# Kernel tuning notes

Measured on AMD Instinct MI355X. Metric: run time of the kernel, lower is better.

The kernel has to match this reference:

```python
import jax, jax.numpy as jnp
import numpy as np

HEAD_DIM = 64
N_HEADS = 12
ROPE_BASE = 10000.0


def _rope_tables(seq_len, head_dim, dtype=jnp.float32):
    half = head_dim // 2
    inv_freq = 1.0 / (ROPE_BASE ** (jnp.arange(0, half, dtype=jnp.float32) / half))
    pos = jnp.arange(seq_len, dtype=jnp.float32)
    freqs = pos[:, None] * inv_freq[None, :]  # (s, half)
    return jnp.cos(freqs).astype(dtype), jnp.sin(freqs).astype(dtype)


def _apply_rope(t, cos, sin):
    # t: (b, h, s, d); rotate-half convention on full head_dim (rope_fraction=1.0)
    d = t.shape[-1]
    t1, t2 = t[..., : d // 2], t[..., d // 2 :]
    cos = cos[None, None, :, :]
    sin = sin[None, None, :, :]
    return jnp.concatenate([t1 * cos - t2 * sin, t1 * sin + t2 * cos], axis=-1)


def setup_inputs() -> dict:
    key = jax.random.key(0)
    ks = jax.random.split(key, 6)
    b, s, d_model = 16, 512, 768
    x = jax.random.normal(ks[0], (b, s, d_model), dtype=jnp.float32)
    chain_ids = jax.random.randint(ks[1], (b, s), 0, 2, dtype=jnp.int32)
    attention_mask = jnp.ones((b, s), dtype=bool)
    inner = N_HEADS * HEAD_DIM
    scale = 0.02
    Wq = jax.random.normal(ks[2], (d_model, inner), dtype=jnp.float32) * scale
    Wk = jax.random.normal(ks[3], (d_model, inner), dtype=jnp.float32) * scale
    Wv = jax.random.normal(ks[4], (d_model, inner), dtype=jnp.float32) * scale
    Wo = jax.random.normal(ks[5], (inner, d_model), dtype=jnp.float32) * scale
    return {"x": x, "chain_ids": chain_ids, "attention_mask": attention_mask,
            "Wq": Wq, "Wk": Wk, "Wv": Wv, "Wo": Wo}


def reference(x, chain_ids, attention_mask, Wq, Wk, Wv, Wo):
    b, s, _ = x.shape
    h, d = N_HEADS, HEAD_DIM
    scale = d ** (-0.5)

    def proj(W):
        return jnp.einsum('bse,ef->bsf', x, W).reshape(b, s, h, d).transpose(0, 2, 1, 3)

    q = proj(Wq)  # (b, h, s, d)
    k = proj(Wk)
    v = proj(Wv)

    cos, sin = _rope_tables(s, d, x.dtype)
    q_rope = _apply_rope(q, cos, sin)
    k_rope = _apply_rope(k, cos, sin)

    scores_intra = jnp.einsum('bhsd,bhtd->bhst', q_rope, k_rope) * scale
    scores_inter = jnp.einsum('bhsd,bhtd->bhst', q, k) * scale

    # intra-chain mask (b, 1, s, s)
    intra = (chain_ids[:, None, :, None] == chain_ids[:, None, None, :])
    merged = jnp.where(intra, scores_intra, scores_inter)

    # additive padding mask (b, 1, 1, s)
    pad = jnp.where(attention_mask[:, None, None, :], 0.0, -jnp.inf).astype(x.dtype)
    merged = merged + pad

    attn = jax.nn.softmax(merged, axis=-1)
    attn = jnp.nan_to_num(attn, nan=0.0)

    out = jnp.einsum('bhst,bhtd->bhsd', attn, v)
    out = out.transpose(0, 2, 1, 3).reshape(b, s, h * d)
    return jnp.einsum('bsf,fe->bse', out, Wo)
```

## Files before the change

### kernel.cpp

```cpp
#include <hip/hip_runtime.h>
#include <stdint.h>
#include <math.h>

#define NB 16
#define NS 512
#define NH 12
#define ND 64
#define NE 768
#define NF 768

typedef __attribute__((ext_vector_type(4))) float  f32x4;
typedef __attribute__((ext_vector_type(8))) short  bf16x8;
typedef __attribute__((ext_vector_type(4))) short  bf16x4;

__device__ __forceinline__ short f2bf(float f) {
    unsigned u = __builtin_bit_cast(unsigned, f);
    u += 0x7FFFu + ((u >> 16) & 1u);
    return (short)(u >> 16);
}
__device__ __forceinline__ float bf2f(short s) {
    unsigned u = ((unsigned)(unsigned short)s) << 16;
    return __builtin_bit_cast(float, u);
}

#define MFMA16(a, b, c) __builtin_amdgcn_mfma_f32_16x16x32_bf16((a), (b), (c), 0, 0, 0)

__device__ __forceinline__ bf16x8 lds_rd8(const short* base, int row, int cb) {
    return *(const bf16x8*)((const char*)base + (((row) * 128 + (cb)) ^ (((row) & 7) << 4)));
}

__global__ __launch_bounds__(256) void mask_probe_kernel(const unsigned char* __restrict__ m,
                                                         int* __restrict__ flag) {
    __shared__ int any;
    if (threadIdx.x == 0) any = 0;
    __syncthreads();
    int acc = 0;
    for (int i = threadIdx.x; i < NB * NS; i += 256) {
        if ((i & 3) && m[i]) acc = 1;
    }
    if (acc) atomicOr(&any, 1);
    __syncthreads();
    if (threadIdx.x == 0) *flag = any;
}

__global__ __launch_bounds__(256) void rope_table_kernel(float* __restrict__ cos_t,
                                                         float* __restrict__ sin_t) {
    int i = blockIdx.x * 256 + threadIdx.x;
    if (i >= NS * 32) return;
    int p = i >> 5;
    int j = i & 31;
    float inv_freq = powf(10000.0f, -(float)j / 32.0f);
    float ang = (float)p * inv_freq;
    cos_t[i] = cosf(ang);
    sin_t[i] = sinf(ang);
}

__global__ __launch_bounds__(256) void convert_x_kernel(const float* __restrict__ x,
                                                        short* __restrict__ xb) {
    int i = (blockIdx.x * 256 + threadIdx.x) * 8;
    if (i >= 8192 * 768) return;
    float4 a = *(const float4*)&x[i];
    float4 b = *(const float4*)&x[i + 4];
    bf16x8 r = { f2bf(a.x), f2bf(a.y), f2bf(a.z), f2bf(a.w),
                 f2bf(b.x), f2bf(b.y), f2bf(b.z), f2bf(b.w) };
    *(bf16x8*)&xb[i] = r;
}

__global__ __launch_bounds__(256) void convert_wt_kernel(
    const float* __restrict__ Wq, const float* __restrict__ Wk,
    const float* __restrict__ Wv, const float* __restrict__ Wo,
    short* __restrict__ Wqt, short* __restrict__ Wkt,
    short* __restrict__ Wvt, short* __restrict__ Wot) {
    const float* W  = (blockIdx.z == 0) ? Wq  : (blockIdx.z == 1) ? Wk  : (blockIdx.z == 2) ? Wv  : Wo;
    short*       Wt = (blockIdx.z == 0) ? Wqt : (blockIdx.z == 1) ? Wkt : (blockIdx.z == 2) ? Wvt : Wot;
    const int k0 = blockIdx.y * 64, n0 = blockIdx.x * 64;
    __shared__ float t[64][65];
    for (int u = threadIdx.x; u < 4096; u += 256) {
        int r = u >> 6, c = u & 63;
        t[r][c] = W[(size_t)(k0 + r) * 768 + n0 + c];
    }
    __syncthreads();
    for (int u = threadIdx.x; u < 4096; u += 256) {
        int c = u >> 6, r = u & 63;
        Wt[(size_t)(n0 + c) * 768 + k0 + r] = f2bf(t[r][c]);
    }
}

__global__ __launch_bounds__(256) void gemm_qkv_kernel(const short* __restrict__ xb,
    const short* __restrict__ Wqt, const short* __restrict__ Wkt, const short* __restrict__ Wvt,
    short* __restrict__ qo, short* __restrict__ ko, short* __restrict__ vo) {
    const int z = blockIdx.z;
    const short* Bt = (z == 0) ? Wqt : (z == 1) ? Wkt : Wvt;
    short*       O  = (z == 0) ? qo  : (z == 1) ? ko  : vo;
    const int n0 = blockIdx.x * 128, m0 = blockIdx.y * 128;
    __shared__ short As[128 * 64], Bs[128 * 64];
    const int tid = threadIdx.x, lane = tid & 63, wave = tid >> 6;
    const int g = lane >> 4, l15 = lane & 15;
    const int wm = wave >> 1, wn = wave & 1;
    f32x4 acc[4][4];
    #pragma unroll
    for (int i = 0; i < 4; ++i)
        #pragma unroll
        for (int j = 0; j < 4; ++j) acc[i][j] = (f32x4){0.f, 0.f, 0.f, 0.f};

    for (int kt = 0; kt < 12; ++kt) {
        __syncthreads();
        const short* Asrc = xb + (size_t)m0 * 768 + kt * 64;
        const short* Bsrc = Bt + (size_t)n0 * 768 + kt * 64;
        #pragma unroll
        for (int p = 0; p < 4; ++p) {
            int u = tid + p * 256;
            int row = u >> 3, slot = u & 7;
            int off = (row * 128 + slot * 16) ^ ((row & 7) << 4);
            *(bf16x8*)((char*)As + off) = *(const bf16x8*)(Asrc + (size_t)row * 768 + slot * 8);
            *(bf16x8*)((char*)Bs + off) = *(const bf16x8*)(Bsrc + (size_t)row * 768 + slot * 8);
        }
        __syncthreads();
        #pragma unroll
        for (int h2 = 0; h2 < 2; ++h2) {
            bf16x8 af[4], bfr[4];
            const int cb = h2 * 64 + g * 16;
            #pragma unroll
            for (int i = 0; i < 4; ++i) {
                af[i]  = lds_rd8(As, wm * 64 + i * 16 + l15, cb);
                bfr[i] = lds_rd8(Bs, wn * 64 + i * 16 + l15, cb);
            }
            #pragma unroll
            for (int i = 0; i < 4; ++i)
                #pragma unroll
                for (int j = 0; j < 4; ++j)
                    acc[i][j] = MFMA16(af[i], bfr[j], acc[i][j]);
        }
    }
    #pragma unroll
    for (int i = 0; i < 4; ++i)
        #pragma unroll
        for (int r = 0; r < 4; ++r) {
            int m = m0 + wm * 64 + i * 16 + g * 4 + r;
            int bb = m >> 9, ss = m & 511;
            #pragma unroll
            for (int j = 0; j < 4; ++j) {
                int n = n0 + wn * 64 + j * 16 + l15;
                int hh = n >> 6, dd = n & 63;
                O[(((size_t)bb * NH + hh) * NS + ss) * ND + dd] = f2bf(acc[i][j][r]);
            }
        }
}

__global__ __launch_bounds__(256) void v_tr_kernel(const short* __restrict__ v,
                                                   short* __restrict__ vt) {
    const int b = blockIdx.z, h = blockIdx.y, s0 = blockIdx.x * 64;
    const size_t base = (((size_t)b * NH + h) * NS + s0) * ND;
    const int tid = threadIdx.x;
    __shared__ short tv[64 * 72];
    #pragma unroll
    for (int p = 0; p < 2; ++p) {
        int u = tid + p * 256;
        int s = u >> 3, d8 = (u & 7) * 8;
        bf16x8 vv = *(const bf16x8*)(v + base + s * 64 + d8);
        #pragma unroll
        for (int j = 0; j < 8; ++j) tv[(d8 + j) * 72 + s] = vv[j];
    }
    __syncthreads();
    const size_t vtb = ((size_t)b * NH + h) * ND * NS + s0;
    #pragma unroll
    for (int p = 0; p < 2; ++p) {
        int u = tid + p * 256;
        int d = u >> 3, s8 = (u & 7) * 8;
        bf16x8 o = *(const bf16x8*)&tv[d * 72 + s8];
        *(bf16x8*)(vt + vtb + (size_t)d * NS + s8) = o;
    }
}

__global__ __launch_bounds__(256) void attn_fused_kernel(
    const short* __restrict__ qr, const short* __restrict__ kr, const short* __restrict__ vt,
    const float* __restrict__ cos_t, const float* __restrict__ sin_t,
    const int* __restrict__ chain, const void* __restrict__ amask,
    const int* __restrict__ mflag, short* __restrict__ aout) {
    const int lid = blockIdx.x;
    const int xcd = lid & 7;
    const int idx = lid >> 3;
    const int qt  = idx & 3;
    const int bh  = xcd * 24 + (idx >> 2);
    const int b = bh / 12, h = bh - (bh / 12) * 12;
    const int q0 = qt * 128;

    __shared__ short SM[20480];
    short* Kr_s = SM;
    short* Kp_s = SM + 4096;
    short* Vt_s = SM + 8192;
    __shared__ __align__(16) int   ck_s[64];
    __shared__ __align__(16) float kb_s[64];

    const int tid = threadIdx.x, lane = tid & 63, wave = tid >> 6;
    const int g = lane >> 4, l15 = lane & 15;
    const int m_u8 = *mflag;
    const size_t bhNS = (size_t)bh * NS;
    char* pb = (char*)(SM + 12288) + wave * 4096;

    const short* qrs = qr + (bhNS + q0) * ND;
    #pragma unroll
    for (int p = 0; p < 4; ++p) {
        int u = tid + p * 256;
        int row = u >> 3, slot = u & 7;
        int off = (row * 128 + slot * 16) ^ ((row & 7) << 4);
        *(bf16x8*)((char*)SM + off) = *(const bf16x8*)(qrs + row * 64 + slot * 8);
    }
    __syncthreads();
    bf16x8 fqr[2][2], fqp[2][2];
    int   cqv[2];
    #pragma unroll
    for (int qg = 0; qg < 2; ++qg) {
        int rrow = wave * 32 + qg * 16 + l15;
        fqr[qg][0] = lds_rd8(SM, rrow, g * 16);
        fqr[qg][1] = lds_rd8(SM, rrow, 64 + g * 16);
        int pos = q0 + rrow;
        float4 c0 = *(const float4*)&cos_t[pos * 32 + g * 8];
        float4 c1 = *(const float4*)&cos_t[pos * 32 + g * 8 + 4];
        float4 s0 = *(const float4*)&sin_t[pos * 32 + g * 8];
        float4 s1 = *(const float4*)&sin_t[pos * 32 + g * 8 + 4];
        float cc[8] = {c0.x, c0.y, c0.z, c0.w, c1.x, c1.y, c1.z, c1.w};
        float ss[8] = {s0.x, s0.y, s0.z, s0.w, s1.x, s1.y, s1.z, s1.w};
        #pragma unroll
        for (int j = 0; j < 8; ++j) {
            float t1 = bf2f(fqr[qg][0][j]), t2 = bf2f(fqr[qg][1][j]);
            fqp[qg][0][j] = f2bf(t1 * cc[j] - t2 * ss[j]);
            fqp[qg][1][j] = f2bf(t1 * ss[j] + t2 * cc[j]);
        }
        cqv[qg] = chain[b * NS + pos];
    }

    float m_run[2] = {-INFINITY, -INFINITY};
    float l_run[2] = {0.f, 0.f};
    f32x4 accO[2][4];
    #pragma unroll
    for (int qg = 0; qg < 2; ++qg)
        #pragma unroll
        for (int t = 0; t < 4; ++t) accO[qg][t] = (f32x4){0.f, 0.f, 0.f, 0.f};

    const short* krb = kr + bhNS * ND;
    const short* vtb = vt + bhNS * ND;

    for (int kv = 0; kv < 8; ++kv) {
        const int k0s = kv * 64;
        __syncthreads();
        {
            int key = tid >> 2, d8 = (tid & 3) * 8;
            const short* krow = krb + (k0s + key) * 64;
            bf16x8 lo = *(const bf16x8*)(krow + d8);
            bf16x8 hi = *(const bf16x8*)(krow + 32 + d8);
            float4 c0 = *(const float4*)&cos_t[(k0s + key) * 32 + d8];
            float4 c1 = *(const float4*)&cos_t[(k0s + key) * 32 + d8 + 4];
            float4 s0 = *(const float4*)&sin_t[(k0s + key) * 32 + d8];
            float4 s1 = *(const float4*)&sin_t[(k0s + key) * 32 + d8 + 4];
            float cc[8] = {c0.x, c0.y, c0.z, c0.w, c1.x, c1.y, c1.z, c1.w};
            float ss[8] = {s0.x, s0.y, s0.z, s0.w, s1.x, s1.y, s1.z, s1.w};
            bf16x8 plo, phi;
            #pragma unroll
            for (int j = 0; j < 8; ++j) {
                float t1 = bf2f(lo[j]), t2 = bf2f(hi[j]);
                plo[j] = f2bf(t1 * cc[j] - t2 * ss[j]);
                phi[j] = f2bf(t1 * ss[j] + t2 * cc[j]);
            }
            int basebyte = key * 128 + d8 * 2;
            int sw = (key & 7) << 4;
            *(bf16x8*)((char*)Kr_s + ((basebyte) ^ sw))      = lo;
            *(bf16x8*)((char*)Kr_s + ((basebyte + 64) ^ sw)) = hi;
            *(bf16x8*)((char*)Kp_s + ((basebyte) ^ sw))      = plo;
            *(bf16x8*)((char*)Kp_s + ((basebyte + 64) ^ sw)) = phi;
        }
        #pragma unroll
        for (int p = 0; p < 2; ++p) {
            int u = tid + p * 256;
            int d = u >> 3, s8 = (u & 7) * 8;
            bf16x8 vv = *(const bf16x8*)(vtb + (size_t)d * NS + k0s + s8);
            *(bf16x8*)((char*)Vt_s + ((d * 128 + s8 * 2) ^ ((d & 7) << 4))) = vv;
        }
        if (tid < 64) {
            int gidx = b * NS + k0s + tid;
            ck_s[tid] = chain[gidx];
            int ok = m_u8 ? (int)((const unsigned char*)amask)[gidx] : ((const int*)amask)[gidx];
            kb_s[tid] = ok ? 0.f : -INFINITY;
        }
        __syncthreads();

        float pm[2][4][4];
        float tmax[2] = {-INFINITY, -INFINITY};
        #pragma unroll
        for (int t = 0; t < 4; ++t) {
            bf16x8 akr0 = lds_rd8(Kr_s, t * 16 + l15, g * 16);
            bf16x8 akr1 = lds_rd8(Kr_s, t * 16 + l15, 64 + g * 16);
            bf16x8 akp0 = lds_rd8(Kp_s, t * 16 + l15, g * 16);
            bf16x8 akp1 = lds_rd8(Kp_s, t * 16 + l15, 64 + g * 16);
            int4   ck4 = *(const int4*)&ck_s[t * 16 + g * 4];
            float4 kb4 = *(const float4*)&kb_s[t * 16 + g * 4];
            const int   ckk[4] = {ck4.x, ck4.y, ck4.z, ck4.w};
            const float kbb[4] = {kb4.x, kb4.y, kb4.z, kb4.w};
            #pragma unroll
            for (int qg = 0; qg < 2; ++qg) {
                f32x4 sr = (f32x4){0.f, 0.f, 0.f, 0.f};
                f32x4 sp = (f32x4){0.f, 0.f, 0.f, 0.f};
                sr = MFMA16(akr0, fqr[qg][0], sr);
                sr = MFMA16(akr1, fqr[qg][1], sr);
                sp = MFMA16(akp0, fqp[qg][0], sp);
                sp = MFMA16(akp1, fqp[qg][1], sp);
                #pragma unroll
                for (int r = 0; r < 4; ++r) {
                    float sv = (cqv[qg] == ckk[r]) ? sp[r] : sr[r];
                    sv = sv * 0.125f + kbb[r];
                    pm[qg][t][r] = sv;
                    tmax[qg] = fmaxf(tmax[qg], sv);
                }
            }
        }

        #pragma unroll
        for (int qg = 0; qg < 2; ++qg) {
            float tm = tmax[qg];
            tm = fmaxf(tm, __shfl_xor(tm, 16));
            tm = fmaxf(tm, __shfl_xor(tm, 32));
            float mnew = fmaxf(m_run[qg], tm);
            float fac, psum = 0.f;
            if (mnew == -INFINITY) {
                fac = 1.f;
                #pragma unroll
                for (int t = 0; t < 4; ++t)
                    #pragma unroll
                    for (int r = 0; r < 4; ++r) pm[qg][t][r] = 0.f;
            } else {
                fac = __expf(m_run[qg] - mnew);
                #pragma unroll
                for (int t = 0; t < 4; ++t)
                    #pragma unroll
                    for (int r = 0; r < 4; ++r) {
                        float p = __expf(pm[qg][t][r] - mnew);
                        pm[qg][t][r] = p;
                        psum += p;
                    }
            }
            psum += __shfl_xor(psum, 16);
            psum += __shfl_xor(psum, 32);
            l_run[qg] = l_run[qg] * fac + psum;
            m_run[qg] = mnew;

            int prow = qg * 16 + l15;
            int psw = (prow & 7) << 4;
            #pragma unroll
            for (int t = 0; t < 4; ++t) {
                bf16x4 pk = { f2bf(pm[qg][t][0]), f2bf(pm[qg][t][1]),
                              f2bf(pm[qg][t][2]), f2bf(pm[qg][t][3]) };
                *(bf16x4*)(pb + ((prow * 128 + t * 32 + g * 8) ^ psw)) = pk;
            }
            float f4[4];
            #pragma unroll
            for (int r = 0; r < 4; ++r) f4[r] = __shfl(fac, g * 4 + r);
            #pragma unroll
            for (int t = 0; t < 4; ++t) {
                f32x4 a = accO[qg][t];
                a[0] *= f4[0]; a[1] *= f4[1]; a[2] *= f4[2]; a[3] *= f4[3];
                accO[qg][t] = a;
            }
            bf16x8 pa0 = *(const bf16x8*)(pb + ((prow * 128 + g * 16) ^ psw));
            bf16x8 pa1 = *(const bf16x8*)(pb + ((prow * 128 + 64 + g * 16) ^ psw));
            #pragma unroll
            for (int dt = 0; dt < 4; ++dt) {
                bf16x8 vb0 = lds_rd8(Vt_s, dt * 16 + l15, g * 16);
                bf16x8 vb1 = lds_rd8(Vt_s, dt * 16 + l15, 64 + g * 16);
                accO[qg][dt] = MFMA16(pa0, vb0, accO[qg][dt]);
                accO[qg][dt] = MFMA16(pa1, vb1, accO[qg][dt]);
            }
        }
    }

    #pragma unroll
    for (int qg = 0; qg < 2; ++qg) {
        float inv[4];
        #pragma unroll
        for (int r = 0; r < 4; ++r) {
            float lv = __shfl(l_run[qg], g * 4 + r);
            inv[r] = (lv > 0.f) ? 1.f / lv : 0.f;
        }
        #pragma unroll
        for (int dt = 0; dt < 4; ++dt)
            #pragma unroll
            for (int r = 0; r < 4; ++r) {
                int row = b * NS + q0 + wave * 32 + qg * 16 + g * 4 + r;
                aout[(size_t)row * NF + h * ND + dt * 16 + l15] = f2bf(accO[qg][dt][r] * inv[r]);
            }
    }
}

__global__ __launch_bounds__(256) void gemm_out_kernel(const short* __restrict__ A,
    const short* __restrict__ Wot, float* __restrict__ out) {
    const int n0 = blockIdx.x * 128, m0 = blockIdx.y * 128;
    __shared__ short As[128 * 64], Bs[128 * 64];
    const int tid = threadIdx.x, lane = tid & 63, wave = tid >> 6;
    const int g = lane >> 4, l15 = lane & 15;
    const int wm = wave >> 1, wn = wave & 1;
    f32x4 acc[4][4];
    #pragma unroll
    for (int i = 0; i < 4; ++i)
        #pragma unroll
        for (int j = 0; j < 4; ++j) acc[i][j] = (f32x4){0.f, 0.f, 0.f, 0.f};

    for (int kt = 0; kt < 12; ++kt) {
        __syncthreads();
        const short* Asrc = A   + (size_t)m0 * 768 + kt * 64;
        const short* Bsrc = Wot + (size_t)n0 * 768 + kt * 64;
        #pragma unroll
        for (int p = 0; p < 4; ++p) {
            int u = tid + p * 256;
            int row = u >> 3, slot = u & 7;
            int off = (row * 128 + slot * 16) ^ ((row & 7) << 4);
            *(bf16x8*)((char*)As + off) = *(const bf16x8*)(Asrc + (size_t)row * 768 + slot * 8);
            *(bf16x8*)((char*)Bs + off) = *(const bf16x8*)(Bsrc + (size_t)row * 768 + slot * 8);
        }
        __syncthreads();
        #pragma unroll
        for (int h2 = 0; h2 < 2; ++h2) {
            bf16x8 af[4], bfr[4];
            const int cb = h2 * 64 + g * 16;
            #pragma unroll
            for (int i = 0; i < 4; ++i) {
                af[i]  = lds_rd8(As, wm * 64 + i * 16 + l15, cb);
                bfr[i] = lds_rd8(Bs, wn * 64 + i * 16 + l15, cb);
            }
            #pragma unroll
            for (int i = 0; i < 4; ++i)
                #pragma unroll
                for (int j = 0; j < 4; ++j)
                    acc[i][j] = MFMA16(af[i], bfr[j], acc[i][j]);
        }
    }
    #pragma unroll
    for (int i = 0; i < 4; ++i)
        #pragma unroll
        for (int r = 0; r < 4; ++r) {
            int m = m0 + wm * 64 + i * 16 + g * 4 + r;
            #pragma unroll
            for (int j = 0; j < 4; ++j) {
                int n = n0 + wn * 64 + j * 16 + l15;
                out[(size_t)m * NE + n] = acc[i][j][r];
            }
        }
}

extern "C" void kernel_launch(void* const* d_in, const int* in_sizes, int n_in,
                              void* d_out, int out_size, void* d_ws, size_t ws_size,
                              hipStream_t stream) {
    const float* x     = (const float*)d_in[0];
    const int*   chain = (const int*)d_in[1];
    const void*  amask = d_in[2];
    const float* Wq = (const float*)d_in[3];
    const float* Wk = (const float*)d_in[4];
    const float* Wv = (const float*)d_in[5];
    const float* Wo = (const float*)d_in[6];
    float* out = (float*)d_out;

    const size_t QSZ = (size_t)NB * NH * NS * ND;
    char* w = (char*)d_ws;
    float* cos_t = (float*)w;  w += (size_t)NS * 32 * 4;
    float* sin_t = (float*)w;  w += (size_t)NS * 32 * 4;
    int*   mflag = (int*)w;    w += 256;
    short* xb    = (short*)w;  w += (size_t)8192 * 768 * 2;
    short* Wqt   = (short*)w;  w += (size_t)768 * 768 * 2;
    short* Wkt   = (short*)w;  w += (size_t)768 * 768 * 2;
    short* Wvt   = (short*)w;  w += (size_t)768 * 768 * 2;
    short* Wot   = (short*)w;  w += (size_t)768 * 768 * 2;
    short* q_raw = (short*)w;  w += QSZ * 2;
    short* k_raw = (short*)w;  w += QSZ * 2;
    short* v_nat = (short*)w;  w += QSZ * 2;
    short* vtr   = (short*)w;  w += QSZ * 2;
    short* aout  = xb;

    mask_probe_kernel<<<dim3(1), dim3(256), 0, stream>>>((const unsigned char*)amask, mflag);
    rope_table_kernel<<<dim3(64), dim3(256), 0, stream>>>(cos_t, sin_t);
    convert_x_kernel<<<dim3(3072), dim3(256), 0, stream>>>(x, xb);
    convert_wt_kernel<<<dim3(12, 12, 4), dim3(256), 0, stream>>>(Wq, Wk, Wv, Wo, Wqt, Wkt, Wvt, Wot);
    gemm_qkv_kernel<<<dim3(6, 64, 3), dim3(256), 0, stream>>>(xb, Wqt, Wkt, Wvt, q_raw, k_raw, v_nat);
    v_tr_kernel<<<dim3(8, 12, 16), dim3(256), 0, stream>>>(v_nat, vtr);
    attn_fused_kernel<<<dim3(768), dim3(256), 0, stream>>>(q_raw, k_raw, vtr, cos_t, sin_t,
                                                           chain, amask, mflag, aout);
    gemm_out_kernel<<<dim3(6, 64), dim3(256), 0, stream>>>(aout, Wot, out);
}
```

Baseline: 164.6 us.

## Use direct global-to-LDS loads, fuse V transpose and prep kernels, retile attention

Merges the mask probe and rope table kernels into one launch. The QKV GEMM now writes V directly in transposed layout, which removes the separate transpose kernel and its buffer. GEMM and attention tile loads use global_load_lds with source-side swizzle, and the MFMA sections are raised with s_setprio. Attention moves to 64 query rows per block (twice as many blocks), folds log2e into the score scale to use exp2f, and skips output rescaling when the running max grows only a little. It also reuses the K tile LDS for P, and the output GEMM is retiled to 64-row blocks. The transposed V stores from the GEMM are strided and uncoalesced, and the lazy rescale trades some numerical exactness for fewer multiplies.

```diff
diff --git a/kernel.cpp b/kernel.cpp
--- a/kernel.cpp
+++ b/kernel.cpp
@@ -13,6 +13,9 @@
 typedef __attribute__((ext_vector_type(8))) short  bf16x8;
 typedef __attribute__((ext_vector_type(4))) short  bf16x4;
 
+#define AS1(p) ((const __attribute__((address_space(1))) unsigned int*)(p))
+#define AS3(p) ((__attribute__((address_space(3))) unsigned int*)(p))
+
 __device__ __forceinline__ short f2bf(float f) {
     unsigned u = __builtin_bit_cast(unsigned, f);
     u += 0x7FFFu + ((u >> 16) & 1u);
@@ -22,6 +25,9 @@
     unsigned u = ((unsigned)(unsigned short)s) << 16;
     return __builtin_bit_cast(float, u);
 }
+__device__ __forceinline__ unsigned pkbf2(float a, float b) {
+    return (unsigned)(unsigned short)f2bf(a) | ((unsigned)(unsigned short)f2bf(b) << 16);
+}
 
 #define MFMA16(a, b, c) __builtin_amdgcn_mfma_f32_16x16x32_bf16((a), (b), (c), 0, 0, 0)
 
@@ -29,26 +35,24 @@
     return *(const bf16x8*)((const char*)base + (((row) * 128 + (cb)) ^ (((row) & 7) << 4)));
 }
 
-__global__ __launch_bounds__(256) void mask_probe_kernel(const unsigned char* __restrict__ m,
-                                                         int* __restrict__ flag) {
-    __shared__ int any;
-    if (threadIdx.x == 0) any = 0;
-    __syncthreads();
-    int acc = 0;
-    for (int i = threadIdx.x; i < NB * NS; i += 256) {
-        if ((i & 3) && m[i]) acc = 1;
-    }
-    if (acc) atomicOr(&any, 1);
-    __syncthreads();
-    if (threadIdx.x == 0) *flag = any;
-}
-
-__global__ __launch_bounds__(256) void rope_table_kernel(float* __restrict__ cos_t,
-                                                         float* __restrict__ sin_t) {
+__global__ __launch_bounds__(256) void prep_kernel(float* __restrict__ cos_t,
+                                                   float* __restrict__ sin_t,
+                                                   const unsigned char* __restrict__ m,
+                                                   int* __restrict__ flag) {
+    if (blockIdx.x == 64) {
+        __shared__ int any;
+        if (threadIdx.x == 0) any = 0;
+        __syncthreads();
+        int acc = 0;
+        for (int i = threadIdx.x; i < NB * NS; i += 256)
+            if ((i & 3) && m[i]) acc = 1;
+        if (acc) atomicOr(&any, 1);
+        __syncthreads();
+        if (threadIdx.x == 0) *flag = any;
+        return;
+    }
     int i = blockIdx.x * 256 + threadIdx.x;
-    if (i >= NS * 32) return;
-    int p = i >> 5;
-    int j = i & 31;
+    int p = i >> 5, j = i & 31;
     float inv_freq = powf(10000.0f, -(float)j / 32.0f);
     float ang = (float)p * inv_freq;
     cos_t[i] = cosf(ang);
@@ -88,10 +92,10 @@
 
 __global__ __launch_bounds__(256) void gemm_qkv_kernel(const short* __restrict__ xb,
     const short* __restrict__ Wqt, const short* __restrict__ Wkt, const short* __restrict__ Wvt,
-    short* __restrict__ qo, short* __restrict__ ko, short* __restrict__ vo) {
+    short* __restrict__ qo, short* __restrict__ ko, short* __restrict__ vto) {
     const int z = blockIdx.z;
     const short* Bt = (z == 0) ? Wqt : (z == 1) ? Wkt : Wvt;
-    short*       O  = (z == 0) ? qo  : (z == 1) ? ko  : vo;
+    short*       O  = (z == 0) ? qo  : (z == 1) ? ko  : vto;
     const int n0 = blockIdx.x * 128, m0 = blockIdx.y * 128;
     __shared__ short As[128 * 64], Bs[128 * 64];
     const int tid = threadIdx.x, lane = tid & 63, wave = tid >> 6;
@@ -105,17 +109,21 @@
 
     for (int kt = 0; kt < 12; ++kt) {
         __syncthreads();
-        const short* Asrc = xb + (size_t)m0 * 768 + kt * 64;
-        const short* Bsrc = Bt + (size_t)n0 * 768 + kt * 64;
+        const char* Asrc = (const char*)(xb + (size_t)m0 * 768 + kt * 64);
+        const char* Bsrc = (const char*)(Bt + (size_t)n0 * 768 + kt * 64);
         #pragma unroll
         for (int p = 0; p < 4; ++p) {
-            int u = tid + p * 256;
-            int row = u >> 3, slot = u & 7;
-            int off = (row * 128 + slot * 16) ^ ((row & 7) << 4);
-            *(bf16x8*)((char*)As + off) = *(const bf16x8*)(Asrc + (size_t)row * 768 + slot * 8);
-            *(bf16x8*)((char*)Bs + off) = *(const bf16x8*)(Bsrc + (size_t)row * 768 + slot * 8);
-        }
-        __syncthreads();
+            int dstoff = (wave * 4 + p) * 1024;
+            int off = dstoff + lane * 16;
+            int row = off >> 7, slot = off & 127;
+            int srcs = slot ^ ((row & 7) << 4);
+            __builtin_amdgcn_global_load_lds(AS1(Asrc + (size_t)row * 1536 + srcs),
+                                             AS3((char*)As + dstoff), 16, 0, 0);
+            __builtin_amdgcn_global_load_lds(AS1(Bsrc + (size_t)row * 1536 + srcs),
+                                             AS3((char*)Bs + dstoff), 16, 0, 0);
+        }
+        __syncthreads();
+        __builtin_amdgcn_s_setprio(1);
         #pragma unroll
         for (int h2 = 0; h2 < 2; ++h2) {
             bf16x8 af[4], bfr[4];
@@ -131,45 +139,25 @@
                 for (int j = 0; j < 4; ++j)
                     acc[i][j] = MFMA16(af[i], bfr[j], acc[i][j]);
         }
+        __builtin_amdgcn_s_setprio(0);
     }
     #pragma unroll
     for (int i = 0; i < 4; ++i)
         #pragma unroll
         for (int r = 0; r < 4; ++r) {
-            int m = m0 + wm * 64 + i * 16 + g * 4 + r;
-            int bb = m >> 9, ss = m & 511;
+            int mm = m0 + wm * 64 + i * 16 + g * 4 + r;
+            int bb = mm >> 9, ss = mm & 511;
             #pragma unroll
             for (int j = 0; j < 4; ++j) {
                 int n = n0 + wn * 64 + j * 16 + l15;
                 int hh = n >> 6, dd = n & 63;
-                O[(((size_t)bb * NH + hh) * NS + ss) * ND + dd] = f2bf(acc[i][j][r]);
-            }
-        }
-}
-
-__global__ __launch_bounds__(256) void v_tr_kernel(const short* __restrict__ v,
-                                                   short* __restrict__ vt) {
-    const int b = blockIdx.z, h = blockIdx.y, s0 = blockIdx.x * 64;
-    const size_t base = (((size_t)b * NH + h) * NS + s0) * ND;
-    const int tid = threadIdx.x;
-    __shared__ short tv[64 * 72];
-    #pragma unroll
-    for (int p = 0; p < 2; ++p) {
-        int u = tid + p * 256;
-        int s = u >> 3, d8 = (u & 7) * 8;
-        bf16x8 vv = *(const bf16x8*)(v + base + s * 64 + d8);
-        #pragma unroll
-        for (int j = 0; j < 8; ++j) tv[(d8 + j) * 72 + s] = vv[j];
-    }
-    __syncthreads();
-    const size_t vtb = ((size_t)b * NH + h) * ND * NS + s0;
-    #pragma unroll
-    for (int p = 0; p < 2; ++p) {
-        int u = tid + p * 256;
-        int d = u >> 3, s8 = (u & 7) * 8;
-        bf16x8 o = *(const bf16x8*)&tv[d * 72 + s8];
-        *(bf16x8*)(vt + vtb + (size_t)d * NS + s8) = o;
-    }
+                short val = f2bf(acc[i][j][r]);
+                if (z == 2)
+                    O[(((size_t)bb * NH + hh) * ND + dd) * NS + ss] = val;
+                else
+                    O[(((size_t)bb * NH + hh) * NS + ss) * ND + dd] = val;
+            }
+        }
 }
 
 __global__ __launch_bounds__(256) void attn_fused_kernel(
@@ -178,17 +166,15 @@
     const int* __restrict__ chain, const void* __restrict__ amask,
     const int* __restrict__ mflag, short* __restrict__ aout) {
     const int lid = blockIdx.x;
-    const int xcd = lid & 7;
-    const int idx = lid >> 3;
-    const int qt  = idx & 3;
-    const int bh  = xcd * 24 + (idx >> 2);
+    const int xcd = lid & 7, idx = lid >> 3;
+    const int qt = idx & 7, bhl = idx >> 3;
+    const int bh = xcd * 24 + bhl;
     const int b = bh / 12, h = bh - (bh / 12) * 12;
-    const int q0 = qt * 128;
-
-    __shared__ short SM[20480];
-    short* Kr_s = SM;
-    short* Kp_s = SM + 4096;
-    short* Vt_s = SM + 8192;
+    const int q0 = qt * 64;
+
+    __shared__ short Kr_s[4096];
+    __shared__ short Kp_s[4096];
+    __shared__ short Vt_s[4096];
     __shared__ __align__(16) int   ck_s[64];
     __shared__ __align__(16) float kb_s[64];
 
@@ -196,25 +182,23 @@
     const int g = lane >> 4, l15 = lane & 15;
     const int m_u8 = *mflag;
     const size_t bhNS = (size_t)bh * NS;
-    char* pb = (char*)(SM + 12288) + wave * 4096;
+    const float SC = 0.18033688011f;
 
     const short* qrs = qr + (bhNS + q0) * ND;
     #pragma unroll
-    for (int p = 0; p < 4; ++p) {
+    for (int p = 0; p < 2; ++p) {
         int u = tid + p * 256;
         int row = u >> 3, slot = u & 7;
         int off = (row * 128 + slot * 16) ^ ((row & 7) << 4);
-        *(bf16x8*)((char*)SM + off) = *(const bf16x8*)(qrs + row * 64 + slot * 8);
+        *(bf16x8*)((char*)Kr_s + off) = *(const bf16x8*)(qrs + row * 64 + slot * 8);
     }
     __syncthreads();
-    bf16x8 fqr[2][2], fqp[2][2];
-    int   cqv[2];
-    #pragma unroll
-    for (int qg = 0; qg < 2; ++qg) {
-        int rrow = wave * 32 + qg * 16 + l15;
-        fqr[qg][0] = lds_rd8(SM, rrow, g * 16);
-        fqr[qg][1] = lds_rd8(SM, rrow, 64 + g * 16);
-        int pos = q0 + rrow;
+    const int qrow = wave * 16 + l15;
+    bf16x8 fqr0 = lds_rd8(Kr_s, qrow, g * 16);
+    bf16x8 fqr1 = lds_rd8(Kr_s, qrow, 64 + g * 16);
+    bf16x8 fqp0, fqp1;
+    {
+        int pos = q0 + qrow;
         float4 c0 = *(const float4*)&cos_t[pos * 32 + g * 8];
         float4 c1 = *(const float4*)&cos_t[pos * 32 + g * 8 + 4];
         float4 s0 = *(const float4*)&sin_t[pos * 32 + g * 8];
@@ -223,23 +207,20 @@
         float ss[8] = {s0.x, s0.y, s0.z, s0.w, s1.x, s1.y, s1.z, s1.w};
         #pragma unroll
         for (int j = 0; j < 8; ++j) {
-            float t1 = bf2f(fqr[qg][0][j]), t2 = bf2f(fqr[qg][1][j]);
-            fqp[qg][0][j] = f2bf(t1 * cc[j] - t2 * ss[j]);
-            fqp[qg][1][j] = f2bf(t1 * ss[j] + t2 * cc[j]);
-        }
-        cqv[qg] = chain[b * NS + pos];
-    }
-
-    float m_run[2] = {-INFINITY, -INFINITY};
-    float l_run[2] = {0.f, 0.f};
-    f32x4 accO[2][4];
-    #pragma unroll
-    for (int qg = 0; qg < 2; ++qg)
-        #pragma unroll
-        for (int t = 0; t < 4; ++t) accO[qg][t] = (f32x4){0.f, 0.f, 0.f, 0.f};
+            float t1 = bf2f(fqr0[j]), t2 = bf2f(fqr1[j]);
+            fqp0[j] = f2bf(t1 * cc[j] - t2 * ss[j]);
+            fqp1[j] = f2bf(t1 * ss[j] + t2 * cc[j]);
+        }
+    }
+    const int cqv = chain[b * NS + q0 + qrow];
+
+    float m_run = -INFINITY, l_run = 0.f;
+    f32x4 accO[4];
+    #pragma unroll
+    for (int t = 0; t < 4; ++t) accO[t] = (f32x4){0.f, 0.f, 0.f, 0.f};
 
     const short* krb = kr + bhNS * ND;
-    const short* vtb = vt + bhNS * ND;
+    const char*  vtb = (const char*)(vt + bhNS * ND);
 
     for (int kv = 0; kv < 8; ++kv) {
         const int k0s = kv * 64;
@@ -271,10 +252,12 @@
         }
         #pragma unroll
         for (int p = 0; p < 2; ++p) {
-            int u = tid + p * 256;
-            int d = u >> 3, s8 = (u & 7) * 8;
-            bf16x8 vv = *(const bf16x8*)(vtb + (size_t)d * NS + k0s + s8);
-            *(bf16x8*)((char*)Vt_s + ((d * 128 + s8 * 2) ^ ((d & 7) << 4))) = vv;
+            int dstoff = (wave * 2 + p) * 1024;
+            int off = dstoff + lane * 16;
+            int d = off >> 7, slot = off & 127;
+            int srcs = slot ^ ((d & 7) << 4);
+            __builtin_amdgcn_global_load_lds(AS1(vtb + (size_t)d * 1024 + k0s * 2 + srcs),
+                                             AS3((char*)Vt_s + dstoff), 16, 0, 0);
         }
         if (tid < 64) {
             int gidx = b * NS + k0s + tid;
@@ -284,163 +267,176 @@
         }
         __syncthreads();
 
-        float pm[2][4][4];
-        float tmax[2] = {-INFINITY, -INFINITY};
+        float pm[4][4];
+        float tm = -INFINITY;
+        __builtin_amdgcn_s_setprio(1);
         #pragma unroll
         for (int t = 0; t < 4; ++t) {
             bf16x8 akr0 = lds_rd8(Kr_s, t * 16 + l15, g * 16);
             bf16x8 akr1 = lds_rd8(Kr_s, t * 16 + l15, 64 + g * 16);
             bf16x8 akp0 = lds_rd8(Kp_s, t * 16 + l15, g * 16);
             bf16x8 akp1 = lds_rd8(Kp_s, t * 16 + l15, 64 + g * 16);
+            f32x4 sr = (f32x4){0.f, 0.f, 0.f, 0.f};
+            f32x4 sp = (f32x4){0.f, 0.f, 0.f, 0.f};
+            sr = MFMA16(akr0, fqr0, sr);
+            sr = MFMA16(akr1, fqr1, sr);
+            sp = MFMA16(akp0, fqp0, sp);
+            sp = MFMA16(akp1, fqp1, sp);
             int4   ck4 = *(const int4*)&ck_s[t * 16 + g * 4];
             float4 kb4 = *(const float4*)&kb_s[t * 16 + g * 4];
             const int   ckk[4] = {ck4.x, ck4.y, ck4.z, ck4.w};
             const float kbb[4] = {kb4.x, kb4.y, kb4.z, kb4.w};
             #pragma unroll
-            for (int qg = 0; qg < 2; ++qg) {
-                f32x4 sr = (f32x4){0.f, 0.f, 0.f, 0.f};
-                f32x4 sp = (f32x4){0.f, 0.f, 0.f, 0.f};
-                sr = MFMA16(akr0, fqr[qg][0], sr);
-                sr = MFMA16(akr1, fqr[qg][1], sr);
-                sp = MFMA16(akp0, fqp[qg][0], sp);
-                sp = MFMA16(akp1, fqp[qg][1], sp);
+            for (int r = 0; r < 4; ++r) {
+                float sv = (cqv == ckk[r]) ? sp[r] : sr[r];
+                sv = sv * SC + kbb[r];
+                pm[t][r] = sv;
+                tm = fmaxf(tm, sv);
+            }
+        }
+        __builtin_amdgcn_s_setprio(0);
+        __syncthreads();
+
+        tm = fmaxf(tm, __shfl_xor(tm, 16));
+        tm = fmaxf(tm, __shfl_xor(tm, 32));
+        bool skip = __all(tm - m_run <= 8.f);
+        float mnew, fac;
+        if (skip) { mnew = m_run; fac = 1.f; }
+        else      { mnew = fmaxf(m_run, tm); fac = exp2f(m_run - mnew); }
+        float psum = 0.f;
+        if (mnew == -INFINITY) {
+            #pragma unroll
+            for (int t = 0; t < 4; ++t)
+                #pragma unroll
+                for (int r = 0; r < 4; ++r) pm[t][r] = 0.f;
+            fac = 1.f;
+        } else {
+            #pragma unroll
+            for (int t = 0; t < 4; ++t)
                 #pragma unroll
                 for (int r = 0; r < 4; ++r) {
-                    float sv = (cqv[qg] == ckk[r]) ? sp[r] : sr[r];
-                    sv = sv * 0.125f + kbb[r];
-                    pm[qg][t][r] = sv;
-                    tmax[qg] = fmaxf(tmax[qg], sv);
+                    float p = exp2f(pm[t][r] - mnew);
+                    pm[t][r] = p;
+                    psum += p;
                 }
-            }
-        }
-
-        #pragma unroll
-        for (int qg = 0; qg < 2; ++qg) {
-            float tm = tmax[qg];
-            tm = fmaxf(tm, __shfl_xor(tm, 16));
-            tm = fmaxf(tm, __shfl_xor(tm, 32));
-            float mnew = fmaxf(m_run[qg], tm);
-            float fac, psum = 0.f;
-            if (mnew == -INFINITY) {
-                fac = 1.f;
-                #pragma unroll
-                for (int t = 0; t < 4; ++t)
-                    #pragma unroll
-                    for (int r = 0; r < 4; ++r) pm[qg][t][r] = 0.f;
-            } else {
-                fac = __expf(m_run[qg] - mnew);
-                #pragma unroll
-                for (int t = 0; t < 4; ++t)
-                    #pragma unroll
-                    for (int r = 0; r < 4; ++r) {
-                        float p = __expf(pm[qg][t][r] - mnew);
-                        pm[qg][t][r] = p;
-                        psum += p;
-                    }
-            }
-            psum += __shfl_xor(psum, 16);
-            psum += __shfl_xor(psum, 32);
-            l_run[qg] = l_run[qg] * fac + psum;
-            m_run[qg] = mnew;
-
-            int prow = qg * 16 + l15;
-            int psw = (prow & 7) << 4;
+        }
+        psum += __shfl_xor(psum, 16);
+        psum += __shfl_xor(psum, 32);
+        l_run = l_run * fac + psum;
+        m_run = mnew;
+
+        char* pwave = (char*)Kr_s + wave * 2048;
+        int psw = (l15 & 7) << 4;
+        #pragma unroll
+        for (int t = 0; t < 4; ++t) {
+            unsigned u0 = pkbf2(pm[t][0], pm[t][1]);
+            unsigned u1 = pkbf2(pm[t][2], pm[t][3]);
+            uint2 pk = {u0, u1};
+            *(uint2*)(pwave + ((l15 * 128 + t * 32 + g * 8) ^ psw)) = pk;
+        }
+        if (!skip) {
+            float f4[4];
+            #pragma unroll
+            for (int r = 0; r < 4; ++r) f4[r] = __shfl(fac, g * 4 + r);
             #pragma unroll
             for (int t = 0; t < 4; ++t) {
-                bf16x4 pk = { f2bf(pm[qg][t][0]), f2bf(pm[qg][t][1]),
-                              f2bf(pm[qg][t][2]), f2bf(pm[qg][t][3]) };
-                *(bf16x4*)(pb + ((prow * 128 + t * 32 + g * 8) ^ psw)) = pk;
-            }
-            float f4[4];
-            #pragma unroll
-            for (int r = 0; r < 4; ++r) f4[r] = __shfl(fac, g * 4 + r);
-            #pragma unroll
-            for (int t = 0; t < 4; ++t) {
-                f32x4 a = accO[qg][t];
+                f32x4 a = accO[t];
                 a[0] *= f4[0]; a[1] *= f4[1]; a[2] *= f4[2]; a[3] *= f4[3];
-                accO[qg][t] = a;
-            }
-            bf16x8 pa0 = *(const bf16x8*)(pb + ((prow * 128 + g * 16) ^ psw));
-            bf16x8 pa1 = *(const bf16x8*)(pb + ((prow * 128 + 64 + g * 16) ^ psw));
-            #pragma unroll
-            for (int dt = 0; dt < 4; ++dt) {
-                bf16x8 vb0 = lds_rd8(Vt_s, dt * 16 + l15, g * 16);
-                bf16x8 vb1 = lds_rd8(Vt_s, dt * 16 + l15, 64 + g * 16);
-                accO[qg][dt] = MFMA16(pa0, vb0, accO[qg][dt]);
-                accO[qg][dt] = MFMA16(pa1, vb1, accO[qg][dt]);
-            }
-        }
-    }
-
-    #pragma unroll
-    for (int qg = 0; qg < 2; ++qg) {
-        float inv[4];
+                accO[t] = a;
+            }
+        }
+        bf16x8 pa0 = *(const bf16x8*)(pwave + ((l15 * 128 + g * 16) ^ psw));
+        bf16x8 pa1 = *(const bf16x8*)(pwave + ((l15 * 128 + 64 + g * 16) ^ psw));
+        __builtin_amdgcn_s_setprio(1);
+        #pragma unroll
+        for (int dt = 0; dt < 4; ++dt) {
+            bf16x8 vb0 = lds_rd8(Vt_s, dt * 16 + l15, g * 16);
+            bf16x8 vb1 = lds_rd8(Vt_s, dt * 16 + l15, 64 + g * 16);
+            accO[dt] = MFMA16(pa0, vb0, accO[dt]);
+            accO[dt] = MFMA16(pa1, vb1, accO[dt]);
+        }
+        __builtin_amdgcn_s_setprio(0);
+    }
+
+    float inv[4];
+    #pragma unroll
+    for (int r = 0; r < 4; ++r) {
+        float lv = __shfl(l_run, g * 4 + r);
+        inv[r] = (lv > 0.f) ? 1.f / lv : 0.f;
+    }
+    #pragma unroll
+    for (int dt = 0; dt < 4; ++dt)
         #pragma unroll
         for (int r = 0; r < 4; ++r) {
-            float lv = __shfl(l_run[qg], g * 4 + r);
-            inv[r] = (lv > 0.f) ? 1.f / lv : 0.f;
-        }
-        #pragma unroll
-        for (int dt = 0; dt < 4; ++dt)
-            #pragma unroll
-            for (int r = 0; r < 4; ++r) {
-                int row = b * NS + q0 + wave * 32 + qg * 16 + g * 4 + r;
-                aout[(size_t)row * NF + h * ND + dt * 16 + l15] = f2bf(accO[qg][dt][r] * inv[r]);
-            }
-    }
+            int row = b * NS + q0 + wave * 16 + g * 4 + r;
+            aout[(size_t)row * NF + h * ND + dt * 16 + l15] = f2bf(accO[dt][r] * inv[r]);
+        }
 }
 
 __global__ __launch_bounds__(256) void gemm_out_kernel(const short* __restrict__ A,
     const short* __restrict__ Wot, float* __restrict__ out) {
-    const int n0 = blockIdx.x * 128, m0 = blockIdx.y * 128;
-    __shared__ short As[128 * 64], Bs[128 * 64];
+    const int n0 = blockIdx.x * 128, m0 = blockIdx.y * 64;
+    __shared__ short As[64 * 64], Bs[128 * 64];
     const int tid = threadIdx.x, lane = tid & 63, wave = tid >> 6;
     const int g = lane >> 4, l15 = lane & 15;
     const int wm = wave >> 1, wn = wave & 1;
-    f32x4 acc[4][4];
-    #pragma unroll
-    for (int i = 0; i < 4; ++i)
+    f32x4 acc[2][4];
+    #pragma unroll
+    for (int i = 0; i < 2; ++i)
         #pragma unroll
         for (int j = 0; j < 4; ++j) acc[i][j] = (f32x4){0.f, 0.f, 0.f, 0.f};
 
     for (int kt = 0; kt < 12; ++kt) {
         __syncthreads();
-        const short* Asrc = A   + (size_t)m0 * 768 + kt * 64;
-        const short* Bsrc = Wot + (size_t)n0 * 768 + kt * 64;
+        const char* Asrc = (const char*)(A   + (size_t)m0 * 768 + kt * 64);
+        const char* Bsrc = (const char*)(Wot + (size_t)n0 * 768 + kt * 64);
+        #pragma unroll
+        for (int p = 0; p < 2; ++p) {
+            int dstoff = (wave * 2 + p) * 1024;
+            int off = dstoff + lane * 16;
+            int row = off >> 7, slot = off & 127;
+            int srcs = slot ^ ((row & 7) << 4);
+            __builtin_amdgcn_global_load_lds(AS1(Asrc + (size_t)row * 1536 + srcs),
+                                             AS3((char*)As + dstoff), 16, 0, 0);
+        }
         #pragma unroll
         for (int p = 0; p < 4; ++p) {
-            int u = tid + p * 256;
-            int row = u >> 3, slot = u & 7;
-            int off = (row * 128 + slot * 16) ^ ((row & 7) << 4);
-            *(bf16x8*)((char*)As + off) = *(const bf16x8*)(Asrc + (size_t)row * 768 + slot * 8);
-            *(bf16x8*)((char*)Bs + off) = *(const bf16x8*)(Bsrc + (size_t)row * 768 + slot * 8);
-        }
-        __syncthreads();
+            int dstoff = (wave * 4 + p) * 1024;
+            int off = dstoff + lane * 16;
+            int row = off >> 7, slot = off & 127;
+            int srcs = slot ^ ((row & 7) << 4);
+            __builtin_amdgcn_global_load_lds(AS1(Bsrc + (size_t)row * 1536 + srcs),
+                                             AS3((char*)Bs + dstoff), 16, 0, 0);
+        }
+        __syncthreads();
+        __builtin_amdgcn_s_setprio(1);
         #pragma unroll
         for (int h2 = 0; h2 < 2; ++h2) {
-            bf16x8 af[4], bfr[4];
+            bf16x8 af[2], bfr[4];
             const int cb = h2 * 64 + g * 16;
             #pragma unroll
-            for (int i = 0; i < 4; ++i) {
-                af[i]  = lds_rd8(As, wm * 64 + i * 16 + l15, cb);
-                bfr[i] = lds_rd8(Bs, wn * 64 + i * 16 + l15, cb);
-            }
-            #pragma unroll
-            for (int i = 0; i < 4; ++i)
+            for (int i = 0; i < 2; ++i)
+                af[i]  = lds_rd8(As, wm * 32 + i * 16 + l15, cb);
+            #pragma unroll
+            for (int j = 0; j < 4; ++j)
+                bfr[j] = lds_rd8(Bs, wn * 64 + j * 16 + l15, cb);
+            #pragma unroll
+            for (int i = 0; i < 2; ++i)
                 #pragma unroll
                 for (int j = 0; j < 4; ++j)
                     acc[i][j] = MFMA16(af[i], bfr[j], acc[i][j]);
         }
-    }
-    #pragma unroll
-    for (int i = 0; i < 4; ++i)
+        __builtin_amdgcn_s_setprio(0);
+    }
+    #pragma unroll
+    for (int i = 0; i < 2; ++i)
         #pragma unroll
         for (int r = 0; r < 4; ++r) {
-            int m = m0 + wm * 64 + i * 16 + g * 4 + r;
+            int mm = m0 + wm * 32 + i * 16 + g * 4 + r;
             #pragma unroll
             for (int j = 0; j < 4; ++j) {
                 int n = n0 + wn * 64 + j * 16 + l15;
-                out[(size_t)m * NE + n] = acc[i][j][r];
+                out[(size_t)mm * NE + n] = acc[i][j][r];
             }
         }
 }
@@ -469,17 +465,15 @@
     short* Wot   = (short*)w;  w += (size_t)768 * 768 * 2;
     short* q_raw = (short*)w;  w += QSZ * 2;
     short* k_raw = (short*)w;  w += QSZ * 2;
-    short* v_nat = (short*)w;  w += QSZ * 2;
     short* vtr   = (short*)w;  w += QSZ * 2;
     short* aout  = xb;
 
-    mask_probe_kernel<<<dim3(1), dim3(256), 0, stream>>>((const unsigned char*)amask, mflag);
-    rope_table_kernel<<<dim3(64), dim3(256), 0, stream>>>(cos_t, sin_t);
+    prep_kernel<<<dim3(65), dim3(256), 0, stream>>>(cos_t, sin_t,
+                                                    (const unsigned char*)amask, mflag);
     convert_x_kernel<<<dim3(3072), dim3(256), 0, stream>>>(x, xb);
     convert_wt_kernel<<<dim3(12, 12, 4), dim3(256), 0, stream>>>(Wq, Wk, Wv, Wo, Wqt, Wkt, Wvt, Wot);
-    gemm_qkv_kernel<<<dim3(6, 64, 3), dim3(256), 0, stream>>>(xb, Wqt, Wkt, Wvt, q_raw, k_raw, v_nat);
-    v_tr_kernel<<<dim3(8, 12, 16), dim3(256), 0, stream>>>(v_nat, vtr);
-    attn_fused_kernel<<<dim3(768), dim3(256), 0, stream>>>(q_raw, k_raw, vtr, cos_t, sin_t,
-                                                           chain, amask, mflag, aout);
-    gemm_out_kernel<<<dim3(6, 64), dim3(256), 0, stream>>>(aout, Wot, out);
-}
+    gemm_qkv_kernel<<<dim3(6, 64, 3), dim3(256), 0, stream>>>(xb, Wqt, Wkt, Wvt, q_raw, k_raw, vtr);
+    attn_fused_kernel<<<dim3(1536), dim3(256), 0, stream>>>(q_raw, k_raw, vtr, cos_t, sin_t,
+                                                            chain, amask, mflag, aout);
+    gemm_out_kernel<<<dim3(6, 128), dim3(256), 0, stream>>>(aout, Wot, out);
+}
```

After: 159.8 us. 1.03x faster.
